# Optimization experiments

Measured on AMD Instinct MI355X. Metric: run time of the kernel, lower is better.

## Reference

```python
import jax, jax.numpy as jnp
import numpy as np

B, CIN, HID, COUT, D, L = 2, 32, 64, 32, 20, 3
D2 = 2 * D
C4, C2 = COUT // 4, COUT // 2


def _conv3(x, W, b):
    # dense stride-1 'SAME' conv == MinkowskiConvolution on occupied set (background is 0)
    y = jax.lax.conv_general_dilated(x, W, (1, 1, 1), 'SAME',
                                     dimension_numbers=('NCDHW', 'OIDHW', 'NCDHW'))
    return y + b[None, :, None, None, None]


def _up(x, W, b):
    # generative conv-transpose, kernel 2 stride 2: out[:, :, 2i+p, 2j+q, 2k+r] = sum_c W[c,:,p,q,r] x[:,c,i,j,k]
    y = jnp.einsum('bcxyz,cdpqr->bdxpyqzr', x, W)
    y = y.reshape(x.shape[0], W.shape[1], 2 * x.shape[2], 2 * x.shape[3], 2 * x.shape[4])
    return y + b[None, :, None, None, None]


def _forward(x_feat, x_occ, target_occ, W_up, b_up, W_conv, b_conv,
             blk_W00, blk_b00, blk_W01, blk_b01, blk_W10, blk_b10,
             blk_W11, blk_b11, blk_W12, blk_b12, W_cls, b_cls, adaptive, rho=1.0):
    b = x_feat.shape[0]
    # occupancy of upsampled coords: every input voxel spawns its 2x2x2 children
    occ_up = jnp.repeat(jnp.repeat(jnp.repeat(x_occ, 2, 1), 2, 2), 2, 3)  # [B,D2,D2,D2]
    m = occ_up[:, None].astype(x_feat.dtype)
    out = jax.nn.relu(_up(x_feat, W_up, b_up) * m)
    out = jax.nn.relu(_conv3(out, W_conv, b_conv) * m)
    # InceptionResNet blocks (PCGCv2 style): two branches, concat, residual add
    for i in range(L):
        o0 = jax.nn.relu(_conv3(out, blk_W00[i], blk_b00[i]) * m)
        o0 = _conv3(o0, blk_W01[i], blk_b01[i]) * m
        o1 = jax.nn.relu(_conv3(out, blk_W10[i], blk_b10[i]) * m)
        o1 = jax.nn.relu(_conv3(o1, blk_W11[i], blk_b11[i]) * m)
        o1 = _conv3(o1, blk_W12[i], blk_b12[i]) * m
        out = jnp.concatenate([o0, o1], axis=1) + out
    out_cls = _conv3(out, W_cls, b_cls) * m
    # get_target_by_sp_tensor: isin(out coords, target coords) -> dense mask intersection
    occ_b = occ_up.astype(bool)
    target = occ_b & target_occ.astype(bool)
    # keep mask (computed under no_grad in torch)
    cls = jax.lax.stop_gradient(out_cls[:, 0]).reshape(b, -1)
    occ_flat = occ_b.reshape(b, -1)
    if adaptive:
        vals = jnp.where(occ_flat, cls, -jnp.inf)
        t_cnt = target_occ.astype(bool).reshape(b, -1).sum(-1)
        k = jnp.minimum(occ_flat.sum(-1), (t_cnt.astype(jnp.float32) * rho).astype(jnp.int32))
        order = jnp.argsort(-vals, axis=-1)
        ranks = jnp.argsort(order, axis=-1)   # descending rank of each voxel
        keep = (ranks < k[:, None]) & occ_flat
    else:
        keep = (cls > 0) & occ_flat
    keep = keep.reshape(occ_b.shape)
    keep = keep | target  # training mode: keep += target
    out_pruned = out * keep[:, None].astype(out.dtype)
    return out_pruned, out_cls, target, keep


def setup_inputs() -> dict:
    key = jax.random.key(0)
    ks = jax.random.split(key, 12)
    s = 0.05
    occ = jax.random.randint(ks[0], (B, D, D, D), 0, 2).astype(jnp.int32)
    x_feat = jax.random.normal(ks[1], (B, CIN, D, D, D), jnp.float32) * occ[:, None].astype(jnp.float32)
    target_occ = jax.random.randint(ks[2], (B, D2, D2, D2), 0, 2).astype(jnp.int32)
    return {
        'x_feat': x_feat, 'x_occ': occ, 'target_occ': target_occ,
        'W_up': jax.random.normal(ks[3], (CIN, HID, 2, 2, 2), jnp.float32) * s,
        'b_up': jnp.zeros((HID,), jnp.float32),
        'W_conv': jax.random.normal(ks[4], (COUT, HID, 3, 3, 3), jnp.float32) * s,
        'b_conv': jnp.zeros((COUT,), jnp.float32),
        'blk_W00': jax.random.normal(ks[5], (L, C4, COUT, 3, 3, 3), jnp.float32) * s,
        'blk_b00': jnp.zeros((L, C4), jnp.float32),
        'blk_W01': jax.random.normal(ks[6], (L, C2, C4, 3, 3, 3), jnp.float32) * s,
        'blk_b01': jnp.zeros((L, C2), jnp.float32),
        'blk_W10': jax.random.normal(ks[7], (L, C4, COUT, 1, 1, 1), jnp.float32) * s,
        'blk_b10': jnp.zeros((L, C4), jnp.float32),
        'blk_W11': jax.random.normal(ks[8], (L, C4, C4, 3, 3, 3), jnp.float32) * s,
        'blk_b11': jnp.zeros((L, C4), jnp.float32),
        'blk_W12': jax.random.normal(ks[9], (L, C2, C4, 1, 1, 1), jnp.float32) * s,
        'blk_b12': jnp.zeros((L, C2), jnp.float32),
        'W_cls': jax.random.normal(ks[10], (1, COUT, 3, 3, 3), jnp.float32) * s,
        'b_cls': jnp.zeros((1,), jnp.float32),
        'adaptive': 1,
    }


def reference(x_feat, x_occ, target_occ, W_up, b_up, W_conv, b_conv,
              blk_W00, blk_b00, blk_W01, blk_b01, blk_W10, blk_b10,
              blk_W11, blk_b11, blk_W12, blk_b12, W_cls, b_cls, adaptive):
    return _forward(x_feat, x_occ, target_occ, W_up, b_up, W_conv, b_conv,
                    blk_W00, blk_b00, blk_W01, blk_b01, blk_W10, blk_b10,
                    blk_W11, blk_b11, blk_W12, blk_b12, W_cls, b_cls, adaptive)
```

## Files before the change

### kernel.cpp

```cpp
#include <hip/hip_runtime.h>
#include <hip/hip_bf16.h>

#define S3 64000
#define NB 2

constexpr int OFF_WUP   = 0;
constexpr int OFF_WCONV = 16384;
constexpr int OFF_W00   = 71680;
constexpr int OFF_W01   = 92416;
constexpr int OFF_W10   = 102784;
constexpr int OFF_W11   = 103552;
constexpr int OFF_W12   = 108736;
constexpr int OFF_ZERO  = 109120;
constexpr int OFF_WCLS  = 109184;
constexpr int NPACK     = 110048;

__device__ const int g_offtab[27] = {
  -1641, -1640, -1639, -1601, -1600, -1599, -1561, -1560, -1559,
    -41,   -40,   -39,    -1,     0,     1,    39,    40,    41,
   1559,  1560,  1561,  1599,  1600,  1601,  1639,  1640,  1641
};

__device__ __forceinline__ int occ_at(const int* __restrict__ x_occ, int b, int s) {
  int d2 = s % 40; int t = s / 40; int d1 = t % 40; int d0 = t / 40;
  return x_occ[b * 8000 + (d0 >> 1) * 400 + (d1 >> 1) * 20 + (d2 >> 1)] != 0;
}

__device__ __forceinline__ unsigned int f2key(float f) {
  unsigned int u = __float_as_uint(f);
  return (u & 0x80000000u) ? ~u : (u | 0x80000000u);
}

__device__ __forceinline__ unsigned int edge_mask27(int d0, int d1, int d2) {
  unsigned int m = 0;
  #pragma unroll
  for (int k0 = 0; k0 < 3; ++k0)
  #pragma unroll
  for (int k1 = 0; k1 < 3; ++k1)
  #pragma unroll
  for (int k2 = 0; k2 < 3; ++k2) {
    bool ok = (k0 == 0 ? (d0 > 0) : (k0 == 2 ? (d0 < 39) : true))
           && (k1 == 0 ? (d1 > 0) : (k1 == 2 ? (d1 < 39) : true))
           && (k2 == 0 ? (d2 > 0) : (k2 == 2 ? (d2 < 39) : true));
    if (ok) m |= 1u << ((k0 * 3 + k1) * 3 + k2);
  }
  return m;
}

__device__ __forceinline__ int swz_xcd(int bid, int G) {
  int q = G >> 3, r = G & 7;
  int x = bid & 7, i = bid >> 3;
  return (x < r ? x * (q + 1) : r * (q + 1) + (x - r) * q) + i;
}

__global__ __launch_bounds__(256)
void pack_all(const float* __restrict__ Wup, const float* __restrict__ Wconv,
              const float* __restrict__ W00, const float* __restrict__ W01,
              const float* __restrict__ W10, const float* __restrict__ W11,
              const float* __restrict__ W12, const float* __restrict__ Wcls,
              float* __restrict__ wp) {
  int i = blockIdx.x * 256 + threadIdx.x;
  if (i < 16384) {
    int tap = i >> 11, rem = i & 2047, c = rem >> 6, d = rem & 63;
    wp[OFF_WUP + i] = Wup[((c << 6) | d) * 8 + tap];
    return;
  }
  i -= 16384;
  if (i < 55296) {
    int tap = i >> 11, c = (i >> 5) & 63, co = i & 31;
    wp[OFF_WCONV + i] = Wconv[(co * 64 + c) * 27 + tap];
    return;
  }
  i -= 55296;
  if (i < 20736) {
    int blk = i / 6912, r = i - blk * 6912;
    int tap = r >> 8, c = (r >> 3) & 31, co = r & 7;
    wp[OFF_W00 + i] = W00[((blk * 8 + co) * 32 + c) * 27 + tap];
    return;
  }
  i -= 20736;
  if (i < 10368) {
    int blk = i / 3456, r = i - blk * 3456;
    int tap = r >> 7, c = (r >> 4) & 7, co = r & 15;
    wp[OFF_W01 + i] = W01[((blk * 16 + co) * 8 + c) * 27 + tap];
    return;
  }
  i -= 10368;
  if (i < 768) {
    int blk = i / 256, r = i - blk * 256;
    int c = r >> 3, co = r & 7;
    wp[OFF_W10 + i] = W10[(blk * 8 + co) * 32 + c];
    return;
  }
  i -= 768;
  if (i < 5184) {
    int blk = i / 1728, r = i - blk * 1728;
    int tap = r >> 6, c = (r >> 3) & 7, co = r & 7;
    wp[OFF_W11 + i] = W11[((blk * 8 + co) * 8 + c) * 27 + tap];
    return;
  }
  i -= 5184;
  if (i < 384) {
    int blk = i / 128, r = i - blk * 128;
    int c = r >> 4, co = r & 15;
    wp[OFF_W12 + i] = W12[(blk * 16 + co) * 8 + c];
    return;
  }
  i -= 384;
  if (i < 64) { wp[OFF_ZERO + i] = 0.f; return; }
  i -= 64;
  if (i < 864) {
    int tap = i / 32, c = i % 32;
    wp[OFF_WCLS + i] = Wcls[c * 27 + tap];
  }
}

__global__ __launch_bounds__(64)
void up_kernel(const float* __restrict__ xf, const float* __restrict__ wup,
               const float* __restrict__ bup, const int* __restrict__ x_occ,
               float* __restrict__ outA) {
  int pv = blockIdx.x * 64 + threadIdx.x;
  int b = pv / 8000, p = pv - b * 8000;
  int p2 = p % 20, t = p / 20, p1 = t % 20, p0 = t / 20;
  int tap = blockIdx.y;
  int O0 = 2 * p0 + (tap >> 2), O1 = 2 * p1 + ((tap >> 1) & 1), O2 = 2 * p2 + (tap & 1);
  int s = O0 * 1600 + O1 * 40 + O2;
  float* op = outA + ((size_t)b * S3 + s) * 64;
  int occ = x_occ[pv];
  float4 z4 = make_float4(0.f, 0.f, 0.f, 0.f);
  if (!occ) {
    #pragma unroll
    for (int i = 0; i < 16; ++i) ((float4*)op)[i] = z4;
    return;
  }
  float acc[64];
  #pragma unroll
  for (int d = 0; d < 64; ++d) acc[d] = bup[d];
  const float* xb = xf + (size_t)b * 32 * 8000 + p;
  const float* wt = wup + tap * 2048;
  #pragma unroll 1
  for (int c = 0; c < 32; ++c) {
    float v = xb[c * 8000];
    const float* w = wt + c * 64;
    #pragma unroll
    for (int d = 0; d < 64; ++d) acc[d] = fmaf(v, w[d], acc[d]);
  }
  #pragma unroll
  for (int i = 0; i < 16; ++i)
    ((float4*)op)[i] = make_float4(fmaxf(acc[4*i],0.f), fmaxf(acc[4*i+1],0.f),
                                   fmaxf(acc[4*i+2],0.f), fmaxf(acc[4*i+3],0.f));
}

__global__ __launch_bounds__(256)
void conv_big(const float* __restrict__ in, const float* __restrict__ w,
              const float* __restrict__ bias, const int* __restrict__ x_occ,
              const float* __restrict__ zpage, float* __restrict__ out) {
  int swl = swz_xcd(blockIdx.x, gridDim.x);
  int tid = swl * 256 + threadIdx.x;
  int b = tid / S3, s = tid - b * S3;
  int d2 = s % 40; int t = s / 40; int d1 = t % 40; int d0 = t / 40;
  int occ = x_occ[b * 8000 + (d0 >> 1) * 400 + (d1 >> 1) * 20 + (d2 >> 1)];
  float* op = out + (size_t)tid * 32;
  float4 z4 = make_float4(0.f, 0.f, 0.f, 0.f);
  if (!occ) {
    #pragma unroll
    for (int i = 0; i < 8; ++i) ((float4*)op)[i] = z4;
    return;
  }
  float acc[32];
  #pragma unroll
  for (int c = 0; c < 32; ++c) acc[c] = bias[c];
  const float* inb = in + (size_t)tid * 64;
  unsigned int m27 = edge_mask27(d0, d1, d2);
  #pragma unroll 1
  for (int tap = 0; tap < 27; ++tap) {
    const float* p = ((m27 >> tap) & 1) ? (inb + g_offtab[tap] * 64) : zpage;
    const float* wt = w + tap * 64 * 32;
    #pragma unroll
    for (int c4 = 0; c4 < 16; ++c4) {
      float4 v = ((const float4*)p)[c4];
      const float* wc = wt + c4 * 4 * 32;
      #pragma unroll
      for (int c = 0; c < 32; ++c) acc[c] = fmaf(v.x, wc[c], acc[c]);
      #pragma unroll
      for (int c = 0; c < 32; ++c) acc[c] = fmaf(v.y, wc[32 + c], acc[c]);
      #pragma unroll
      for (int c = 0; c < 32; ++c) acc[c] = fmaf(v.z, wc[64 + c], acc[c]);
      #pragma unroll
      for (int c = 0; c < 32; ++c) acc[c] = fmaf(v.w, wc[96 + c], acc[c]);
    }
  }
  #pragma unroll
  for (int c = 0; c < 32; ++c) acc[c] = fmaxf(acc[c], 0.f);
  #pragma unroll
  for (int c = 0; c < 8; ++c)
    ((float4*)op)[c] = make_float4(acc[4*c], acc[4*c+1], acc[4*c+2], acc[4*c+3]);
}

__global__ __launch_bounds__(256)
void conv_k1(const float* __restrict__ in, const float* __restrict__ w3,
             const float* __restrict__ w1, const float* __restrict__ b3,
             const float* __restrict__ b1, const int* __restrict__ x_occ,
             const float* __restrict__ zpage, float* __restrict__ T0o,
             float* __restrict__ T1o) {
  int tid = blockIdx.x * 256 + threadIdx.x;
  int b = tid / S3, s = tid - b * S3;
  int d2 = s % 40; int t = s / 40; int d1 = t % 40; int d0 = t / 40;
  int occ = x_occ[b * 8000 + (d0 >> 1) * 400 + (d1 >> 1) * 20 + (d2 >> 1)];
  float* o0 = T0o + (size_t)tid * 8;
  float* o1 = T1o + (size_t)tid * 8;
  float4 z4 = make_float4(0.f, 0.f, 0.f, 0.f);
  if (!occ) {
    ((float4*)o0)[0] = z4; ((float4*)o0)[1] = z4;
    ((float4*)o1)[0] = z4; ((float4*)o1)[1] = z4;
    return;
  }
  float a0[8], a1[8];
  #pragma unroll
  for (int co = 0; co < 8; ++co) { a0[co] = b3[co]; a1[co] = b1[co]; }
  const float* inb = in + (size_t)tid * 32;
  #pragma unroll
  for (int c4 = 0; c4 < 8; ++c4) {
    float4 v = ((const float4*)inb)[c4];
    const float* wc = w1 + c4 * 4 * 8;
    #pragma unroll
    for (int co = 0; co < 8; ++co) a1[co] = fmaf(v.x, wc[co], a1[co]);
    #pragma unroll
    for (int co = 0; co < 8; ++co) a1[co] = fmaf(v.y, wc[8 + co], a1[co]);
    #pragma unroll
    for (int co = 0; co < 8; ++co) a1[co] = fmaf(v.z, wc[16 + co], a1[co]);
    #pragma unroll
    for (int co = 0; co < 8; ++co) a1[co] = fmaf(v.w, wc[24 + co], a1[co]);
  }
  unsigned int m27 = edge_mask27(d0, d1, d2);
  #pragma unroll 1
  for (int tap = 0; tap < 27; ++tap) {
    const float* p = ((m27 >> tap) & 1) ? (inb + g_offtab[tap] * 32) : zpage;
    const float* wt = w3 + tap * 32 * 8;
    #pragma unroll
    for (int c4 = 0; c4 < 8; ++c4) {
      float4 v = ((const float4*)p)[c4];
      const float* wc = wt + c4 * 4 * 8;
      #pragma unroll
      for (int co = 0; co < 8; ++co) a0[co] = fmaf(v.x, wc[co], a0[co]);
      #pragma unroll
      for (int co = 0; co < 8; ++co) a0[co] = fmaf(v.y, wc[8 + co], a0[co]);
      #pragma unroll
      for (int co = 0; co < 8; ++co) a0[co] = fmaf(v.z, wc[16 + co], a0[co]);
      #pragma unroll
      for (int co = 0; co < 8; ++co) a0[co] = fmaf(v.w, wc[24 + co], a0[co]);
    }
  }
  ((float4*)o0)[0] = make_float4(fmaxf(a0[0],0.f), fmaxf(a0[1],0.f), fmaxf(a0[2],0.f), fmaxf(a0[3],0.f));
  ((float4*)o0)[1] = make_float4(fmaxf(a0[4],0.f), fmaxf(a0[5],0.f), fmaxf(a0[6],0.f), fmaxf(a0[7],0.f));
  ((float4*)o1)[0] = make_float4(fmaxf(a1[0],0.f), fmaxf(a1[1],0.f), fmaxf(a1[2],0.f), fmaxf(a1[3],0.f));
  ((float4*)o1)[1] = make_float4(fmaxf(a1[4],0.f), fmaxf(a1[5],0.f), fmaxf(a1[6],0.f), fmaxf(a1[7],0.f));
}

__global__ __launch_bounds__(256)
void conv_k3f(const float* __restrict__ t0, const float* __restrict__ t1,
              const float* __restrict__ resid, const float* __restrict__ w01,
              const float* __restrict__ w11, const float* __restrict__ w12,
              const float* __restrict__ bb01, const float* __restrict__ bb11,
              const float* __restrict__ bb12, const int* __restrict__ x_occ,
              const float* __restrict__ zpage, float* __restrict__ nxt) {
  int tid = blockIdx.x * 256 + threadIdx.x;
  int b = tid / S3, s = tid - b * S3;
  int d2 = s % 40; int t = s / 40; int d1 = t % 40; int d0 = t / 40;
  int occ = x_occ[b * 8000 + (d0 >> 1) * 400 + (d1 >> 1) * 20 + (d2 >> 1)];
  float* op = nxt + (size_t)tid * 32;
  float4 z4 = make_float4(0.f, 0.f, 0.f, 0.f);
  if (!occ) {
    #pragma unroll
    for (int i = 0; i < 8; ++i) ((float4*)op)[i] = z4;
    return;
  }
  float a[16], t2[8];
  #pragma unroll
  for (int co = 0; co < 16; ++co) a[co] = bb01[co];
  #pragma unroll
  for (int co = 0; co < 8; ++co) t2[co] = bb11[co];
  const float* t0b = t0 + (size_t)tid * 8;
  const float* t1b = t1 + (size_t)tid * 8;
  unsigned int m27 = edge_mask27(d0, d1, d2);
  #pragma unroll 1
  for (int tap = 0; tap < 27; ++tap) {
    bool ok = (m27 >> tap) & 1;
    const float* p0 = ok ? (t0b + g_offtab[tap] * 8) : zpage;
    const float* p1 = ok ? (t1b + g_offtab[tap] * 8) : zpage;
    const float* wt0 = w01 + tap * 128;
    #pragma unroll
    for (int c4 = 0; c4 < 2; ++c4) {
      float4 v = ((const float4*)p0)[c4];
      const float* wc = wt0 + c4 * 64;
      #pragma unroll
      for (int co = 0; co < 16; ++co) a[co] = fmaf(v.x, wc[co], a[co]);
      #pragma unroll
      for (int co = 0; co < 16; ++co) a[co] = fmaf(v.y, wc[16 + co], a[co]);
      #pragma unroll
      for (int co = 0; co < 16; ++co) a[co] = fmaf(v.z, wc[32 + co], a[co]);
      #pragma unroll
      for (int co = 0; co < 16; ++co) a[co] = fmaf(v.w, wc[48 + co], a[co]);
    }
    const float* wt1 = w11 + tap * 64;
    #pragma unroll
    for (int c4 = 0; c4 < 2; ++c4) {
      float4 v = ((const float4*)p1)[c4];
      const float* wc = wt1 + c4 * 32;
      #pragma unroll
      for (int co = 0; co < 8; ++co) t2[co] = fmaf(v.x, wc[co], t2[co]);
      #pragma unroll
      for (int co = 0; co < 8; ++co) t2[co] = fmaf(v.y, wc[8 + co], t2[co]);
      #pragma unroll
      for (int co = 0; co < 8; ++co) t2[co] = fmaf(v.z, wc[16 + co], t2[co]);
      #pragma unroll
      for (int co = 0; co < 8; ++co) t2[co] = fmaf(v.w, wc[24 + co], t2[co]);
    }
  }
  #pragma unroll
  for (int co = 0; co < 8; ++co) t2[co] = fmaxf(t2[co], 0.f);
  float a1[16];
  #pragma unroll
  for (int co = 0; co < 16; ++co) a1[co] = bb12[co];
  #pragma unroll
  for (int c = 0; c < 8; ++c) {
    #pragma unroll
    for (int co = 0; co < 16; ++co) a1[co] = fmaf(t2[c], w12[c * 16 + co], a1[co]);
  }
  const float* rb = resid + (size_t)tid * 32;
  float o[32];
  #pragma unroll
  for (int co = 0; co < 16; ++co) { o[co] = a[co]; o[16 + co] = a1[co]; }
  #pragma unroll
  for (int q = 0; q < 8; ++q) {
    float4 r = ((const float4*)rb)[q];
    o[4*q] += r.x; o[4*q+1] += r.y; o[4*q+2] += r.z; o[4*q+3] += r.w;
  }
  #pragma unroll
  for (int q = 0; q < 8; ++q)
    ((float4*)op)[q] = make_float4(o[4*q], o[4*q+1], o[4*q+2], o[4*q+3]);
}

__global__ __launch_bounds__(256)
void cls_kernel(const float* __restrict__ in, const float* __restrict__ w,
                const float* __restrict__ bias, const int* __restrict__ x_occ,
                const float* __restrict__ zpage, float* __restrict__ CLSo) {
  int tid = blockIdx.x * 256 + threadIdx.x;
  int b = tid / S3, s = tid - b * S3;
  int d2 = s % 40; int t = s / 40; int d1 = t % 40; int d0 = t / 40;
  int occ = x_occ[b * 8000 + (d0 >> 1) * 400 + (d1 >> 1) * 20 + (d2 >> 1)];
  if (!occ) { CLSo[tid] = 0.f; return; }
  float acc = bias[0];
  const float* inb = in + (size_t)tid * 32;
  unsigned int m27 = edge_mask27(d0, d1, d2);
  #pragma unroll 1
  for (int tap = 0; tap < 27; ++tap) {
    const float* p = ((m27 >> tap) & 1) ? (inb + g_offtab[tap] * 32) : zpage;
    const float* wt = w + tap * 32;
    #pragma unroll
    for (int c4 = 0; c4 < 8; ++c4) {
      float4 v = ((const float4*)p)[c4];
      acc = fmaf(v.x, wt[4*c4], acc);
      acc = fmaf(v.y, wt[4*c4+1], acc);
      acc = fmaf(v.z, wt[4*c4+2], acc);
      acc = fmaf(v.w, wt[4*c4+3], acc);
    }
  }
  CLSo[tid] = acc;
}

__global__ __launch_bounds__(256)
void sel_zero(int* __restrict__ hist) {
  int i = blockIdx.x * 256 + threadIdx.x;
  int n = 3 * NB * 65536 + NB * 16;
  for (int j = i; j < n; j += 512 * 256) hist[j] = 0;
}

__global__ __launch_bounds__(256)
void sel_hist1(const float* __restrict__ cls, const int* __restrict__ x_occ,
               const int* __restrict__ tgt, unsigned int* __restrict__ key,
               int* __restrict__ hist, int* __restrict__ sel) {
  int tid = blockIdx.x * 256 + threadIdx.x;
  int b = tid / S3, s = tid - b * S3;
  int occ = occ_at(x_occ, b, s);
  int tg = tgt[tid] != 0;
  unsigned int kk = occ ? f2key(cls[tid]) : 0u;
  key[tid] = kk;
  if (occ) atomicAdd(&hist[b * 65536 + (kk >> 16)], 1);
  unsigned long long bo = __ballot(occ);
  unsigned long long bt = __ballot(tg);
  if ((threadIdx.x & 63) == 0) {
    atomicAdd(&sel[b * 16 + 0], (int)__popcll(bo));
    atomicAdd(&sel[b * 16 + 1], (int)__popcll(bt));
  }
}

__global__ __launch_bounds__(256)
void sel_hist2(const unsigned int* __restrict__ key, const int* __restrict__ x_occ,
               int* __restrict__ hist, const int* __restrict__ sel) {
  int tid = blockIdx.x * 256 + threadIdx.x;
  int b = tid / S3, s = tid - b * S3;
  int B1 = sel[b * 16 + 4];
  if (B1 < 0) return;
  if (!occ_at(x_occ, b, s)) return;
  unsigned int kk = key[tid];
  if ((int)(kk >> 16) == B1) atomicAdd(&hist[(NB + b) * 65536 + (kk & 0xFFFFu)], 1);
}

__global__ __launch_bounds__(256)
void sel_hist3(const unsigned int* __restrict__ key, const int* __restrict__ x_occ,
               int* __restrict__ hist, const int* __restrict__ sel) {
  int tid = blockIdx.x * 256 + threadIdx.x;
  int b = tid / S3, s = tid - b * S3;
  int B1 = sel[b * 16 + 4];
  if (B1 < 0) return;
  if (!occ_at(x_occ, b, s)) return;
  unsigned int k32 = ((unsigned)B1 << 16) | (unsigned)sel[b * 16 + 5];
  if (key[tid] == k32) atomicAdd(&hist[(2 * NB + b) * 65536 + (65535 - s)], 1);
}

__global__ __launch_bounds__(256)
void sel_scan(int* __restrict__ hist, int* __restrict__ sel,
              const int* __restrict__ adaptive_flag, int phase) {
  int b = blockIdx.x;
  int* sb = sel + b * 16;
  __shared__ int chunk[256];
  __shared__ int s_active, s_rank;
  int t = threadIdx.x;
  if (t == 0) {
    int active = 1;
    if (phase == 0) {
      int k = min(sb[0], sb[1]);
      sb[2] = k; sb[3] = k;
      if (!adaptive_flag[0] || k == 0) {
        sb[4] = -1000000;
        *(unsigned long long*)(sb + 6) = ~0ull;
        active = 0;
      }
    } else if (sb[4] == -1000000) {
      active = 0;
    }
    s_active = active; s_rank = sb[3];
  }
  __syncthreads();
  if (!s_active) return;
  const int* hb = hist + (phase * NB + b) * 65536;
  int sum = 0;
  #pragma unroll 4
  for (int v = 0; v < 256; ++v) sum += hb[t * 256 + v];
  chunk[t] = sum;
  __syncthreads();
  if (t == 0) {
    int r = s_rank, acc = 0, C = 0;
    for (int c = 255; c >= 0; --c) {
      if (acc + chunk[c] >= r) { C = c; r -= acc; break; }
      acc += chunk[c];
    }
    int B = C * 256;
    acc = 0;
    for (int v = 255; v >= 0; --v) {
      int h = hb[C * 256 + v];
      if (acc + h >= r) { B = C * 256 + v; r -= acc; break; }
      acc += h;
    }
    if (phase == 0)      { sb[4] = B; sb[3] = r; }
    else if (phase == 1) { sb[5] = B; sb[3] = r; }
    else {
      unsigned long long T = ((unsigned long long)sb[4] << 16) | (unsigned)sb[5];
      T = (T << 16) | (unsigned)B;
      *(unsigned long long*)(sb + 6) = T;
    }
  }
}

__global__ __launch_bounds__(256)
void emit_prune(const float* __restrict__ cls, const unsigned int* __restrict__ key,
                const int* __restrict__ x_occ, const int* __restrict__ tgt,
                const int* __restrict__ adaptive_flag, const int* __restrict__ sel,
                const float* __restrict__ cur, float* __restrict__ dout) {
  int tid = blockIdx.x * 256 + threadIdx.x;
  int b = tid / S3, s = tid - b * S3;
  int occ = occ_at(x_occ, b, s);
  int tg = occ && (tgt[tid] != 0);
  float c = cls[tid];
  bool kp;
  if (adaptive_flag[0]) {
    unsigned long long T = *(const unsigned long long*)(sel + b * 16 + 6);
    unsigned long long k48 = ((unsigned long long)key[tid] << 16) | (unsigned)(65535 - s);
    kp = occ && (k48 >= T);
  } else {
    kp = occ && (c > 0.f);
  }
  kp = kp || tg;
  float* tail = dout + (size_t)NB * 32 * S3;
  tail[tid] = c;
  tail[NB * S3 + tid] = tg ? 1.f : 0.f;
  tail[2 * NB * S3 + tid] = kp ? 1.f : 0.f;
  float sc = kp ? 1.f : 0.f;
  const float4* ip = (const float4*)(cur + (size_t)tid * 32);
  float* ob = dout + (size_t)b * 32 * S3 + s;
  #pragma unroll
  for (int i = 0; i < 8; ++i) {
    float4 q = ip[i];
    ob[(4 * i) * S3] = q.x * sc; ob[(4 * i + 1) * S3] = q.y * sc;
    ob[(4 * i + 2) * S3] = q.z * sc; ob[(4 * i + 3) * S3] = q.w * sc;
  }
}

extern "C" void kernel_launch(void* const* d_in, const int* in_sizes, int n_in,
                              void* d_out, int out_size, void* d_ws, size_t ws_size,
                              hipStream_t stream) {
  const float* x_feat    = (const float*)d_in[0];
  const int*   x_occ     = (const int*)d_in[1];
  const int*   target_oc = (const int*)d_in[2];
  const float* W_up   = (const float*)d_in[3];
  const float* b_up   = (const float*)d_in[4];
  const float* W_conv = (const float*)d_in[5];
  const float* b_conv = (const float*)d_in[6];
  const float* W00 = (const float*)d_in[7];
  const float* b00 = (const float*)d_in[8];
  const float* W01 = (const float*)d_in[9];
  const float* b01 = (const float*)d_in[10];
  const float* W10 = (const float*)d_in[11];
  const float* b10 = (const float*)d_in[12];
  const float* W11 = (const float*)d_in[13];
  const float* b11 = (const float*)d_in[14];
  const float* W12 = (const float*)d_in[15];
  const float* b12 = (const float*)d_in[16];
  const float* W_cls = (const float*)d_in[17];
  const float* b_cls = (const float*)d_in[18];
  const int*   adaptive = (const int*)d_in[19];

  float* ws = (float*)d_ws;
  float* wp = ws;
  float* zp = wp + OFF_ZERO;
  float* A  = ws + (1 << 17);
  float* B0 = A + (size_t)NB * S3 * 64;
  float* B1 = B0 + (size_t)NB * S3 * 32;
  float* T0 = A;
  float* T1 = T0 + (size_t)NB * S3 * 8;
  float* CLS = T1 + (size_t)NB * S3 * 8;
  unsigned int* KEY = (unsigned int*)(CLS + (size_t)NB * S3);
  int* HIST = (int*)(KEY + (size_t)NB * S3);
  int* SEL  = HIST + 3 * NB * 65536;

  float* outf = (float*)d_out;

  pack_all<<<(NPACK + 255) / 256, 256, 0, stream>>>(W_up, W_conv, W00, W01, W10, W11, W12, W_cls, wp);
  up_kernel<<<dim3(250, 8), 64, 0, stream>>>(x_feat, wp + OFF_WUP, b_up, x_occ, A);
  conv_big<<<500, 256, 0, stream>>>(A, wp + OFF_WCONV, b_conv, x_occ, zp, B0);

  float* cur = B0;
  float* nxt = B1;
  for (int i = 0; i < 3; ++i) {
    conv_k1<<<500, 256, 0, stream>>>(cur, wp + OFF_W00 + i * 6912, wp + OFF_W10 + i * 256,
                                     b00 + i * 8, b10 + i * 8, x_occ, zp, T0, T1);
    conv_k3f<<<500, 256, 0, stream>>>(T0, T1, cur, wp + OFF_W01 + i * 3456, wp + OFF_W11 + i * 1728,
                                      wp + OFF_W12 + i * 128, b01 + i * 16, b11 + i * 8, b12 + i * 16,
                                      x_occ, zp, nxt);
    float* tswap = cur; cur = nxt; nxt = tswap;
  }
  cls_kernel<<<500, 256, 0, stream>>>(cur, wp + OFF_WCLS, b_cls, x_occ, zp, CLS);

  sel_zero<<<512, 256, 0, stream>>>(HIST);
  sel_hist1<<<500, 256, 0, stream>>>(CLS, x_occ, target_oc, KEY, HIST, SEL);
  sel_scan<<<NB, 256, 0, stream>>>(HIST, SEL, adaptive, 0);
  sel_hist2<<<500, 256, 0, stream>>>(KEY, x_occ, HIST, SEL);
  sel_scan<<<NB, 256, 0, stream>>>(HIST, SEL, adaptive, 1);
  sel_hist3<<<500, 256, 0, stream>>>(KEY, x_occ, HIST, SEL);
  sel_scan<<<NB, 256, 0, stream>>>(HIST, SEL, adaptive, 2);
  emit_prune<<<500, 256, 0, stream>>>(CLS, KEY, x_occ, target_oc, adaptive, SEL, cur, outf);
}
```

Baseline: 787.6 us.

## Split big conv output channels across grid, template it, unroll tap loops by two

Replaces conv_big with a templated conv3_cl that computes 16 of the 32 output channels per thread, launched on a 500x2 grid, so each thread holds half as many accumulators and twice as many threads run. The XCD block swizzle is dropped. Tap loops in all conv kernels are unrolled by two to expose more memory-level parallelism. The cost is that every input neighbourhood is read twice, once per channel half, and unrolling may raise register pressure.

```diff
diff --git a/kernel.cpp b/kernel.cpp
--- a/kernel.cpp
+++ b/kernel.cpp
@@ -45,12 +45,6 @@
     if (ok) m |= 1u << ((k0 * 3 + k1) * 3 + k2);
   }
   return m;
-}
-
-__device__ __forceinline__ int swz_xcd(int bid, int G) {
-  int q = G >> 3, r = G & 7;
-  int x = bid & 7, i = bid >> 3;
-  return (x < r ? x * (q + 1) : r * (q + 1) + (x - r) * q) + i;
 }
 
 __global__ __launch_bounds__(256)
@@ -151,49 +145,52 @@
                                    fmaxf(acc[4*i+2],0.f), fmaxf(acc[4*i+3],0.f));
 }
 
-__global__ __launch_bounds__(256)
-void conv_big(const float* __restrict__ in, const float* __restrict__ w,
+template<int CIN, int COUT, int WS, bool RELU>
+__global__ __launch_bounds__(256)
+void conv3_cl(const float* __restrict__ in, const float* __restrict__ w,
               const float* __restrict__ bias, const int* __restrict__ x_occ,
-              const float* __restrict__ zpage, float* __restrict__ out) {
-  int swl = swz_xcd(blockIdx.x, gridDim.x);
-  int tid = swl * 256 + threadIdx.x;
+              const float* __restrict__ zpage, float* __restrict__ out, int outc) {
+  int tid = blockIdx.x * 256 + threadIdx.x;
   int b = tid / S3, s = tid - b * S3;
   int d2 = s % 40; int t = s / 40; int d1 = t % 40; int d0 = t / 40;
   int occ = x_occ[b * 8000 + (d0 >> 1) * 400 + (d1 >> 1) * 20 + (d2 >> 1)];
-  float* op = out + (size_t)tid * 32;
+  int cb = blockIdx.y * COUT;
+  float* op = out + (size_t)tid * outc + cb;
   float4 z4 = make_float4(0.f, 0.f, 0.f, 0.f);
   if (!occ) {
     #pragma unroll
-    for (int i = 0; i < 8; ++i) ((float4*)op)[i] = z4;
-    return;
-  }
-  float acc[32];
-  #pragma unroll
-  for (int c = 0; c < 32; ++c) acc[c] = bias[c];
-  const float* inb = in + (size_t)tid * 64;
+    for (int i = 0; i < COUT / 4; ++i) ((float4*)op)[i] = z4;
+    return;
+  }
+  const float* wb = w + cb;
+  const float* bb = bias + cb;
+  float acc[COUT];
+  #pragma unroll
+  for (int c = 0; c < COUT; ++c) acc[c] = bb[c];
+  const float* inb = in + (size_t)tid * CIN;
   unsigned int m27 = edge_mask27(d0, d1, d2);
-  #pragma unroll 1
+  #pragma unroll 2
   for (int tap = 0; tap < 27; ++tap) {
-    const float* p = ((m27 >> tap) & 1) ? (inb + g_offtab[tap] * 64) : zpage;
-    const float* wt = w + tap * 64 * 32;
-    #pragma unroll
-    for (int c4 = 0; c4 < 16; ++c4) {
+    const float* p = ((m27 >> tap) & 1) ? (inb + g_offtab[tap] * CIN) : zpage;
+    const float* wt = wb + tap * CIN * WS;
+    #pragma unroll
+    for (int c4 = 0; c4 < CIN / 4; ++c4) {
       float4 v = ((const float4*)p)[c4];
-      const float* wc = wt + c4 * 4 * 32;
-      #pragma unroll
-      for (int c = 0; c < 32; ++c) acc[c] = fmaf(v.x, wc[c], acc[c]);
-      #pragma unroll
-      for (int c = 0; c < 32; ++c) acc[c] = fmaf(v.y, wc[32 + c], acc[c]);
-      #pragma unroll
-      for (int c = 0; c < 32; ++c) acc[c] = fmaf(v.z, wc[64 + c], acc[c]);
-      #pragma unroll
-      for (int c = 0; c < 32; ++c) acc[c] = fmaf(v.w, wc[96 + c], acc[c]);
-    }
-  }
-  #pragma unroll
-  for (int c = 0; c < 32; ++c) acc[c] = fmaxf(acc[c], 0.f);
-  #pragma unroll
-  for (int c = 0; c < 8; ++c)
+      const float* wc = wt + c4 * 4 * WS;
+      #pragma unroll
+      for (int c = 0; c < COUT; ++c) acc[c] = fmaf(v.x, wc[c], acc[c]);
+      #pragma unroll
+      for (int c = 0; c < COUT; ++c) acc[c] = fmaf(v.y, wc[WS + c], acc[c]);
+      #pragma unroll
+      for (int c = 0; c < COUT; ++c) acc[c] = fmaf(v.z, wc[2 * WS + c], acc[c]);
+      #pragma unroll
+      for (int c = 0; c < COUT; ++c) acc[c] = fmaf(v.w, wc[3 * WS + c], acc[c]);
+    }
+  }
+  #pragma unroll
+  for (int c = 0; c < COUT; ++c) if (RELU) acc[c] = fmaxf(acc[c], 0.f);
+  #pragma unroll
+  for (int c = 0; c < COUT / 4; ++c)
     ((float4*)op)[c] = make_float4(acc[4*c], acc[4*c+1], acc[4*c+2], acc[4*c+3]);
 }
 
@@ -233,7 +230,7 @@
     for (int co = 0; co < 8; ++co) a1[co] = fmaf(v.w, wc[24 + co], a1[co]);
   }
   unsigned int m27 = edge_mask27(d0, d1, d2);
-  #pragma unroll 1
+  #pragma unroll 2
   for (int tap = 0; tap < 27; ++tap) {
     const float* p = ((m27 >> tap) & 1) ? (inb + g_offtab[tap] * 32) : zpage;
     const float* wt = w3 + tap * 32 * 8;
@@ -283,7 +280,7 @@
   const float* t0b = t0 + (size_t)tid * 8;
   const float* t1b = t1 + (size_t)tid * 8;
   unsigned int m27 = edge_mask27(d0, d1, d2);
-  #pragma unroll 1
+  #pragma unroll 2
   for (int tap = 0; tap < 27; ++tap) {
     bool ok = (m27 >> tap) & 1;
     const float* p0 = ok ? (t0b + g_offtab[tap] * 8) : zpage;
@@ -353,7 +350,7 @@
   float acc = bias[0];
   const float* inb = in + (size_t)tid * 32;
   unsigned int m27 = edge_mask27(d0, d1, d2);
-  #pragma unroll 1
+  #pragma unroll 2
   for (int tap = 0; tap < 27; ++tap) {
     const float* p = ((m27 >> tap) & 1) ? (inb + g_offtab[tap] * 32) : zpage;
     const float* wt = w + tap * 32;
@@ -548,7 +545,7 @@
 
   pack_all<<<(NPACK + 255) / 256, 256, 0, stream>>>(W_up, W_conv, W00, W01, W10, W11, W12, W_cls, wp);
   up_kernel<<<dim3(250, 8), 64, 0, stream>>>(x_feat, wp + OFF_WUP, b_up, x_occ, A);
-  conv_big<<<500, 256, 0, stream>>>(A, wp + OFF_WCONV, b_conv, x_occ, zp, B0);
+  conv3_cl<64, 16, 32, true><<<dim3(500, 2), 256, 0, stream>>>(A, wp + OFF_WCONV, b_conv, x_occ, zp, B0, 32);
 
   float* cur = B0;
   float* nxt = B1;
```

Measured after the change: 641.4 us. 1.23x faster.
